# Optimization experiments

Measured on AMD Instinct MI355X. Metric: run time of the kernel, lower is better.

## Reference

```python
import jax, jax.numpy as jnp
import numpy as np

B, T, D_MODEL, N_HEAD = 2, 2048, 1024, 16
HEAD_DIM = D_MODEL // N_HEAD


def setup_inputs() -> dict:
    key = jax.random.key(0)
    ks = jax.random.split(key, 4)
    s = 0.02
    return {
        "x": jax.random.normal(ks[0], (B, T, D_MODEL), dtype=jnp.float32),
        "freqs_cis": jnp.zeros((T, HEAD_DIM // 2), dtype=jnp.float32),  # unused under ALiBi
        "Wq": jax.random.normal(ks[1], (D_MODEL, D_MODEL), dtype=jnp.float32) * s,
        "bq": jnp.zeros((D_MODEL,), dtype=jnp.float32),
        "Wkv": jax.random.normal(ks[2], (2 * D_MODEL, D_MODEL), dtype=jnp.float32) * s,
        "bkv": jnp.zeros((2 * D_MODEL,), dtype=jnp.float32),
        "Wo": jax.random.normal(ks[3], (D_MODEL, D_MODEL), dtype=jnp.float32) * s,
        "bo": jnp.zeros((D_MODEL,), dtype=jnp.float32),
    }


def reference(x, freqs_cis, Wq, bq, Wkv, bkv, Wo, bo):
    Bb, Tt, C = x.shape
    H, Dh = N_HEAD, HEAD_DIM
    # projections (torch Linear: x @ W^T + b)
    q = (x @ Wq.T + bq).reshape(Bb, Tt, H, Dh).transpose(0, 2, 1, 3)      # [B,H,T,Dh]
    kv = (x @ Wkv.T + bkv).reshape(Bb, Tt, 2, H, Dh).transpose(2, 0, 3, 1, 4)
    k, v = kv[0], kv[1]                                                    # [B,H,T,Dh]
    scores = jnp.einsum('bhqd,bhkd->bhqk', q, k) * (1.0 / np.sqrt(Dh))
    # ALiBi: linear slopes (1/H ... 1.0), bias = slope * (j - i)
    slopes = jnp.arange(1, H + 1, dtype=jnp.float32) / H                   # [H]
    pos = jnp.arange(Tt, dtype=jnp.float32)
    dist = pos[None, :] - pos[:, None]                                     # [T,T], j - i
    scores = scores + slopes[:, None, None] * dist[None]                   # broadcast over B
    # causal mask (upper triangle -> -inf)
    causal = pos[:, None] >= pos[None, :]                                  # [T,T] keep-mask
    scores = jnp.where(causal[None, None], scores, -jnp.inf)
    attn = jax.nn.softmax(scores, axis=-1)
    y = jnp.einsum('bhqk,bhkd->bhqd', attn, v)                             # [B,H,T,Dh]
    y = y.transpose(0, 2, 1, 3).reshape(Bb, Tt, C)
    return y @ Wo.T + bo
```

## Files before the change

### kernel.cpp

```cpp
#include <hip/hip_runtime.h>

typedef unsigned short u16;
typedef unsigned int u32;
typedef __bf16 bf16x8 __attribute__((ext_vector_type(8)));
typedef unsigned short u16x8 __attribute__((ext_vector_type(8)));
typedef float f32x4 __attribute__((ext_vector_type(4)));

#define KEY(r) ((((r) ^ ((r) >> 3)) & 7) << 3)
#define GP 72
#define VKEY(d) ((((d) >> 3) & 7) << 3)

static __device__ __forceinline__ u16 f2b(float f) {
  union { float f; unsigned u; } x; x.f = f;
  unsigned r = x.u + 0x7FFFu + ((x.u >> 16) & 1u);
  return (u16)(r >> 16);
}

static __device__ __forceinline__ bf16x8 ld_frag(const u16* p) {
  union { u16x8 s; bf16x8 b; } u;
  u.s = *reinterpret_cast<const u16x8*>(p);
  return u.b;
}

__global__ __launch_bounds__(256) void cvt_f32_bf16(const float* __restrict__ in,
                                                    u16* __restrict__ out, int n4) {
  int i = blockIdx.x * 256 + threadIdx.x;
  if (i >= n4) return;
  float4 v = reinterpret_cast<const float4*>(in)[i];
  ushort4 o;
  o.x = f2b(v.x); o.y = f2b(v.y); o.z = f2b(v.z); o.w = f2b(v.w);
  reinterpret_cast<ushort4*>(out)[i] = o;
}

template <bool OUT_BF16, int BN>
static __device__ __forceinline__ void gemm_body(
    const u16* __restrict__ A, const u16* __restrict__ Bt,
    const float* __restrict__ bias, void* __restrict__ outp,
    int N, int K, int row0, int col0, float scale) {
  constexpr int NF = BN / 32;
  __shared__ alignas(16) u16 As[128 * 64];
  __shared__ alignas(16) u16 Bs[BN * 64];
  const int tid = threadIdx.x, wid = tid >> 6, lane = tid & 63;
  const int wr = wid >> 1, wc = wid & 1;
  const int lr = lane >> 3;
  const int lc = (lane & 7) * 8;
  const int frow = lane & 15, fk = (lane >> 4) * 8;
  f32x4 acc[4][NF] = {};

  for (int k0 = 0; k0 < K; k0 += 64) {
    __syncthreads();
#pragma unroll
    for (int t = 0; t < 4; ++t) {
      const int r = wid * 32 + t * 8 + lr;
      __builtin_amdgcn_global_load_lds(
          (const __attribute__((address_space(1))) unsigned int*)(
              A + (size_t)(row0 + r) * K + k0 + (lc ^ KEY(r))),
          (__attribute__((address_space(3))) unsigned int*)(As + (wid * 32 + t * 8) * 64),
          16, 0, 0);
    }
#pragma unroll
    for (int t = 0; t < NF; ++t) {
      const int r = wid * (BN / 4) + t * 8 + lr;
      __builtin_amdgcn_global_load_lds(
          (const __attribute__((address_space(1))) unsigned int*)(
              Bt + (size_t)(col0 + r) * K + k0 + (lc ^ KEY(r))),
          (__attribute__((address_space(3))) unsigned int*)(Bs + (wid * (BN / 4) + t * 8) * 64),
          16, 0, 0);
    }
    __syncthreads();
#pragma unroll
    for (int ks = 0; ks < 2; ++ks) {
      bf16x8 a[4], b[NF];
#pragma unroll
      for (int m = 0; m < 4; ++m) {
        const int r = wr * 64 + m * 16 + frow;
        a[m] = ld_frag(&As[r * 64 + ((ks * 32 + fk) ^ KEY(r))]);
      }
#pragma unroll
      for (int n = 0; n < NF; ++n) {
        const int r = wc * (BN / 2) + n * 16 + frow;
        b[n] = ld_frag(&Bs[r * 64 + ((ks * 32 + fk) ^ KEY(r))]);
      }
#pragma unroll
      for (int m = 0; m < 4; ++m)
#pragma unroll
        for (int n = 0; n < NF; ++n)
          acc[m][n] = __builtin_amdgcn_mfma_f32_16x16x32_bf16(a[m], b[n], acc[m][n], 0, 0, 0);
    }
  }
  const int colL = lane & 15, rb = (lane >> 4) * 4;
#pragma unroll
  for (int n = 0; n < NF; ++n) {
    const int gc = col0 + wc * (BN / 2) + n * 16 + colL;
    const float bv = bias[gc];
#pragma unroll
    for (int m = 0; m < 4; ++m)
#pragma unroll
      for (int r = 0; r < 4; ++r) {
        const int gr = row0 + wr * 64 + m * 16 + rb + r;
        const float v = (acc[m][n][r] + bv) * scale;
        if constexpr (OUT_BF16)
          reinterpret_cast<u16*>(outp)[(size_t)gr * N + gc] = f2b(v);
        else
          reinterpret_cast<float*>(outp)[(size_t)gr * N + gc] = v;
      }
  }
}

__global__ __launch_bounds__(256) void gemm_qkv(
    const u16* __restrict__ xb, const u16* __restrict__ wqb,
    const u16* __restrict__ wkvb, const float* __restrict__ bq,
    const float* __restrict__ bkv, u16* __restrict__ qb, u16* __restrict__ kvb) {
  const int row0 = blockIdx.x * 128;
  const int by = blockIdx.y;
  const u16* Bt; const float* bias; u16* out; int N, col0; float scale;
  if (by < 8) { Bt = wqb;  bias = bq;  out = qb;  N = 1024; col0 = by * 128;      scale = 0.125f; }
  else        { Bt = wkvb; bias = bkv; out = kvb; N = 2048; col0 = (by - 8) * 128; scale = 1.0f; }
  gemm_body<true, 128>(xb, Bt, bias, out, N, 1024, row0, col0, scale);
}

__global__ __launch_bounds__(256) void gemm_o(
    const u16* __restrict__ yb, const u16* __restrict__ wob,
    const float* __restrict__ bo, float* __restrict__ out) {
  gemm_body<false, 64>(yb, wob, bo, out, 1024, 1024, blockIdx.x * 128, blockIdx.y * 64, 1.0f);
}

__global__ __launch_bounds__(256) void attn_kernel(
    const u16* __restrict__ qb,
    const u16* __restrict__ kvb,
    u16* __restrict__ yb,
    int T) {
  const int C = 1024;
  const int bh = blockIdx.x;
  const int qt = (int)gridDim.y - 1 - (int)blockIdx.y;
  const int b = bh >> 4, h = bh & 15;
  const float slope = (float)(h + 1) * 0.0625f;
  const int tid = threadIdx.x, wid = tid >> 6, lane = tid & 63;
  const int qBase = qt * 64;

  __shared__ alignas(16) u16 Ks[64 * GP];
  __shared__ alignas(16) u16 Vt[64 * GP];
  __shared__ alignas(16) u32 Pl[4][16 * 40];

  const int qc = lane & 15;
  const int g  = lane >> 4;
  const int g4 = g * 4;
  const int fk = g * 8;

  const int q_row = qBase + wid * 16 + qc;
  const u16* qp = qb + (size_t)(b * T + q_row) * C + h * 64;
  const bf16x8 aq0 = ld_frag(qp + fk);
  const bf16x8 aq1 = ld_frag(qp + 32 + fk);
  const int qg = q_row;

  float m_q = -1e30f, l_q = 0.f;
  f32x4 accO[4] = {};

  const int sr = tid >> 3;
  const int sc = (tid & 7) * 8;

  for (int kt = 0; kt <= qt; ++kt) {
    const int kBase = kt * 64;
    __syncthreads();
    {
      const size_t g0 = (size_t)(b * T + kBase + sr) * 2048 + h * 64 + sc;
      const size_t g1 = (size_t)(b * T + kBase + sr + 32) * 2048 + h * 64 + sc;
      *reinterpret_cast<int4*>(&Ks[sr * GP + sc]) = *reinterpret_cast<const int4*>(&kvb[g0]);
      *reinterpret_cast<int4*>(&Ks[(sr + 32) * GP + sc]) = *reinterpret_cast<const int4*>(&kvb[g1]);
      int4 v0 = *reinterpret_cast<const int4*>(&kvb[g0 + 1024]);
      int4 v1 = *reinterpret_cast<const int4*>(&kvb[g1 + 1024]);
      const u16* p0 = reinterpret_cast<const u16*>(&v0);
      const u16* p1 = reinterpret_cast<const u16*>(&v1);
      const int kx = VKEY(sc);
#pragma unroll
      for (int j = 0; j < 8; ++j) {
        const int d = sc + j;
        Vt[d * GP + (sr ^ kx)] = p0[j];
        Vt[d * GP + ((sr + 32) ^ kx)] = p1[j];
      }
    }
    __syncthreads();

    f32x4 accS[4] = {};
#pragma unroll
    for (int n = 0; n < 4; ++n) {
      bf16x8 bk0 = ld_frag(&Ks[(n * 16 + qc) * GP + fk]);
      accS[n] = __builtin_amdgcn_mfma_f32_16x16x32_bf16(bk0, aq0, accS[n], 0, 0, 0);
      bf16x8 bk1 = ld_frag(&Ks[(n * 16 + qc) * GP + 32 + fk]);
      accS[n] = __builtin_amdgcn_mfma_f32_16x16x32_bf16(bk1, aq1, accS[n], 0, 0, 0);
    }

    float tmax = -1e30f;
#pragma unroll
    for (int n = 0; n < 4; ++n) {
      const int kgn = kBase + n * 16 + g4;
#pragma unroll
      for (int r = 0; r < 4; ++r) {
        const int kg = kgn + r;
        float v = fmaf(slope, (float)kg, accS[n][r]);
        v = (kg > qg) ? -1e30f : v;
        accS[n][r] = v;
        tmax = fmaxf(tmax, v);
      }
    }
    tmax = fmaxf(tmax, __shfl_xor(tmax, 16));
    tmax = fmaxf(tmax, __shfl_xor(tmax, 32));
    const float newm = fmaxf(m_q, tmax);
    const float corr = __expf(m_q - newm);
    m_q = newm;
    float psum = 0.f;
#pragma unroll
    for (int n = 0; n < 4; ++n)
#pragma unroll
      for (int r = 0; r < 4; ++r) {
        const float p = __expf(accS[n][r] - newm);
        accS[n][r] = p;
        psum += p;
      }
    psum += __shfl_xor(psum, 16);
    psum += __shfl_xor(psum, 32);
    l_q = l_q * corr + psum;

    u32* Pw = &Pl[wid][qc * 40];
#pragma unroll
    for (int n = 0; n < 4; ++n) {
      union { float f; u32 u; } a0, a1, a2, a3;
      a0.f = accS[n][0]; a1.f = accS[n][1]; a2.f = accS[n][2]; a3.f = accS[n][3];
      u32 w0 = (a0.u >> 16) | (a1.u & 0xFFFF0000u);
      u32 w1 = (a2.u >> 16) | (a3.u & 0xFFFF0000u);
      *reinterpret_cast<uint2*>(&Pw[8 * n + 2 * g]) = uint2{w0, w1};
    }

    float corr4[4];
#pragma unroll
    for (int r = 0; r < 4; ++r) corr4[r] = __shfl(corr, g4 + r);
#pragma unroll
    for (int n = 0; n < 4; ++n)
#pragma unroll
      for (int r = 0; r < 4; ++r) accO[n][r] *= corr4[r];

#pragma unroll
    for (int ks = 0; ks < 2; ++ks) {
      uint4 pv4 = *reinterpret_cast<const uint4*>(&Pl[wid][qc * 40 + 16 * ks + g4]);
      union { uint4 q; u16x8 s; bf16x8 bv; } ap; ap.q = pv4;
#pragma unroll
      for (int n = 0; n < 4; ++n) {
        const int d = n * 16 + qc;
        bf16x8 bv = ld_frag(&Vt[d * GP + ((ks * 32 + fk) ^ VKEY(d))]);
        accO[n] = __builtin_amdgcn_mfma_f32_16x16x32_bf16(ap.bv, bv, accO[n], 0, 0, 0);
      }
    }
  }

  float inv4[4];
#pragma unroll
  for (int r = 0; r < 4; ++r) inv4[r] = 1.0f / __shfl(l_q, g4 + r);
#pragma unroll
  for (int r = 0; r < 4; ++r) {
    const int qg2 = qBase + wid * 16 + g4 + r;
    u16* yrow = yb + (size_t)(b * T + qg2) * C + h * 64;
#pragma unroll
    for (int n = 0; n < 4; ++n) yrow[n * 16 + qc] = f2b(accO[n][r] * inv4[r]);
  }
}

extern "C" void kernel_launch(void* const* d_in, const int* in_sizes, int n_in,
                              void* d_out, int out_size, void* d_ws, size_t ws_size,
                              hipStream_t stream) {
  const float* x   = (const float*)d_in[0];
  const float* Wq  = (const float*)d_in[2];
  const float* bq  = (const float*)d_in[3];
  const float* Wkv = (const float*)d_in[4];
  const float* bkv = (const float*)d_in[5];
  const float* Wo  = (const float*)d_in[6];
  const float* bo  = (const float*)d_in[7];
  float* out = (float*)d_out;

  const int B = 2, T = 2048, C = 1024;
  const int M = B * T;

  char* ws = (char*)d_ws;
  u16* xb   = (u16*)(ws + 0);
  u16* wqb  = (u16*)(ws + 8388608);
  u16* wkvb = (u16*)(ws + 10485760);
  u16* wob  = (u16*)(ws + 14680064);
  u16* qb   = (u16*)(ws + 16777216);
  u16* kvb  = (u16*)(ws + 25165824);
  u16* yb   = (u16*)(ws + 41943040);

  cvt_f32_bf16<<<(M * C / 4 + 255) / 256, 256, 0, stream>>>(x, xb, M * C / 4);
  cvt_f32_bf16<<<(C * C / 4 + 255) / 256, 256, 0, stream>>>(Wq, wqb, C * C / 4);
  cvt_f32_bf16<<<(2 * C * C / 4 + 255) / 256, 256, 0, stream>>>(Wkv, wkvb, 2 * C * C / 4);
  cvt_f32_bf16<<<(C * C / 4 + 255) / 256, 256, 0, stream>>>(Wo, wob, C * C / 4);

  gemm_qkv<<<dim3(M / 128, 8 + 16), 256, 0, stream>>>(xb, wqb, wkvb, bq, bkv, qb, kvb);
  attn_kernel<<<dim3(B * 16, T / 64), 256, 0, stream>>>(qb, kvb, yb, T);
  gemm_o<<<dim3(M / 128, C / 64), 256, 0, stream>>>(yb, wob, bo, out);
}
```

Measured before the change: 213.8 us.

## Fuse conversion launches and widen attention KV tiles with register prefetch

The four fp32-to-bf16 conversion launches are merged into one kernel that picks its source and destination by index range. The attention kernel now processes 128 keys per iteration instead of 64, halving the number of barrier/softmax-rescale rounds. It also prefetches the next K/V tile into registers while the current one is computed. This raises register and LDS use, which may lower occupancy, and computes more masked scores on the diagonal tile. It also changes the LDS padding strides for Vt and the P buffer.

Result: slower. 231.8 us (+8.4%).

```diff
diff --git a/kernel.cpp b/kernel.cpp
--- a/kernel.cpp
+++ b/kernel.cpp
@@ -7,7 +7,9 @@
 typedef float f32x4 __attribute__((ext_vector_type(4)));
 
 #define KEY(r) ((((r) ^ ((r) >> 3)) & 7) << 3)
-#define GP 72
+#define GPK 72
+#define GPV 136
+#define PLP 65
 #define VKEY(d) ((((d) >> 3) & 7) << 3)
 
 static __device__ __forceinline__ u16 f2b(float f) {
@@ -22,14 +24,22 @@
   return u.b;
 }
 
-__global__ __launch_bounds__(256) void cvt_f32_bf16(const float* __restrict__ in,
-                                                    u16* __restrict__ out, int n4) {
-  int i = blockIdx.x * 256 + threadIdx.x;
-  if (i >= n4) return;
-  float4 v = reinterpret_cast<const float4*>(in)[i];
+__global__ __launch_bounds__(256) void cvt_all(
+    const float* __restrict__ x, const float* __restrict__ Wq,
+    const float* __restrict__ Wkv, const float* __restrict__ Wo,
+    u16* __restrict__ xb, u16* __restrict__ wqb,
+    u16* __restrict__ wkvb, u16* __restrict__ wob) {
+  const int i = blockIdx.x * 256 + threadIdx.x;
+  const float* in; u16* out; int base;
+  if (i < 1048576)      { in = x;   out = xb;   base = 0; }
+  else if (i < 1310720) { in = Wq;  out = wqb;  base = 1048576; }
+  else if (i < 1835008) { in = Wkv; out = wkvb; base = 1310720; }
+  else                  { in = Wo;  out = wob;  base = 1835008; }
+  const int j = i - base;
+  float4 v = reinterpret_cast<const float4*>(in)[j];
   ushort4 o;
   o.x = f2b(v.x); o.y = f2b(v.y); o.z = f2b(v.z); o.w = f2b(v.w);
-  reinterpret_cast<ushort4*>(out)[i] = o;
+  reinterpret_cast<ushort4*>(out)[j] = o;
 }
 
 template <bool OUT_BF16, int BN>
@@ -138,9 +148,9 @@
   const int tid = threadIdx.x, wid = tid >> 6, lane = tid & 63;
   const int qBase = qt * 64;
 
-  __shared__ alignas(16) u16 Ks[64 * GP];
-  __shared__ alignas(16) u16 Vt[64 * GP];
-  __shared__ alignas(16) u32 Pl[4][16 * 40];
+  __shared__ alignas(16) u16 Ks[128 * GPK];
+  __shared__ alignas(16) u16 Vt[64 * GPV];
+  __shared__ alignas(16) u32 Pl[4][16 * PLP];
 
   const int qc = lane & 15;
   const int g  = lane >> 4;
@@ -158,41 +168,56 @@
 
   const int sr = tid >> 3;
   const int sc = (tid & 7) * 8;
-
-  for (int kt = 0; kt <= qt; ++kt) {
-    const int kBase = kt * 64;
+  const int kx = VKEY(sc);
+
+  const int nt = (qt + 2) >> 1;
+
+  int4 kreg[4], vreg[4];
+#pragma unroll
+  for (int t = 0; t < 4; ++t) {
+    const int r = sr + 32 * t;
+    const size_t gaddr = (size_t)(b * T + r) * 2048 + h * 64 + sc;
+    kreg[t] = *reinterpret_cast<const int4*>(&kvb[gaddr]);
+    vreg[t] = *reinterpret_cast<const int4*>(&kvb[gaddr + 1024]);
+  }
+
+  for (int kt = 0; kt < nt; ++kt) {
+    const int kBase = kt * 128;
     __syncthreads();
-    {
-      const size_t g0 = (size_t)(b * T + kBase + sr) * 2048 + h * 64 + sc;
-      const size_t g1 = (size_t)(b * T + kBase + sr + 32) * 2048 + h * 64 + sc;
-      *reinterpret_cast<int4*>(&Ks[sr * GP + sc]) = *reinterpret_cast<const int4*>(&kvb[g0]);
-      *reinterpret_cast<int4*>(&Ks[(sr + 32) * GP + sc]) = *reinterpret_cast<const int4*>(&kvb[g1]);
-      int4 v0 = *reinterpret_cast<const int4*>(&kvb[g0 + 1024]);
-      int4 v1 = *reinterpret_cast<const int4*>(&kvb[g1 + 1024]);
-      const u16* p0 = reinterpret_cast<const u16*>(&v0);
-      const u16* p1 = reinterpret_cast<const u16*>(&v1);
-      const int kx = VKEY(sc);
+#pragma unroll
+    for (int t = 0; t < 4; ++t) {
+      const int r = sr + 32 * t;
+      *reinterpret_cast<int4*>(&Ks[r * GPK + sc]) = kreg[t];
+      const u16* pv = reinterpret_cast<const u16*>(&vreg[t]);
 #pragma unroll
       for (int j = 0; j < 8; ++j) {
         const int d = sc + j;
-        Vt[d * GP + (sr ^ kx)] = p0[j];
-        Vt[d * GP + ((sr + 32) ^ kx)] = p1[j];
+        Vt[d * GPV + (r ^ kx)] = pv[j];
       }
     }
     __syncthreads();
-
-    f32x4 accS[4] = {};
-#pragma unroll
-    for (int n = 0; n < 4; ++n) {
-      bf16x8 bk0 = ld_frag(&Ks[(n * 16 + qc) * GP + fk]);
+    if (kt + 1 < nt) {
+#pragma unroll
+      for (int t = 0; t < 4; ++t) {
+        const int r = sr + 32 * t;
+        const size_t gaddr = (size_t)(b * T + kBase + 128 + r) * 2048 + h * 64 + sc;
+        kreg[t] = *reinterpret_cast<const int4*>(&kvb[gaddr]);
+        vreg[t] = *reinterpret_cast<const int4*>(&kvb[gaddr + 1024]);
+      }
+    }
+
+    f32x4 accS[8] = {};
+#pragma unroll
+    for (int n = 0; n < 8; ++n) {
+      bf16x8 bk0 = ld_frag(&Ks[(n * 16 + qc) * GPK + fk]);
       accS[n] = __builtin_amdgcn_mfma_f32_16x16x32_bf16(bk0, aq0, accS[n], 0, 0, 0);
-      bf16x8 bk1 = ld_frag(&Ks[(n * 16 + qc) * GP + 32 + fk]);
+      bf16x8 bk1 = ld_frag(&Ks[(n * 16 + qc) * GPK + 32 + fk]);
       accS[n] = __builtin_amdgcn_mfma_f32_16x16x32_bf16(bk1, aq1, accS[n], 0, 0, 0);
     }
 
     float tmax = -1e30f;
 #pragma unroll
-    for (int n = 0; n < 4; ++n) {
+    for (int n = 0; n < 8; ++n) {
       const int kgn = kBase + n * 16 + g4;
 #pragma unroll
       for (int r = 0; r < 4; ++r) {
@@ -210,7 +235,7 @@
     m_q = newm;
     float psum = 0.f;
 #pragma unroll
-    for (int n = 0; n < 4; ++n)
+    for (int n = 0; n < 8; ++n)
 #pragma unroll
       for (int r = 0; r < 4; ++r) {
         const float p = __expf(accS[n][r] - newm);
@@ -221,9 +246,9 @@
     psum += __shfl_xor(psum, 32);
     l_q = l_q * corr + psum;
 
-    u32* Pw = &Pl[wid][qc * 40];
-#pragma unroll
-    for (int n = 0; n < 4; ++n) {
+    u32* Pw = &Pl[wid][qc * PLP];
+#pragma unroll
+    for (int n = 0; n < 8; ++n) {
       union { float f; u32 u; } a0, a1, a2, a3;
       a0.f = accS[n][0]; a1.f = accS[n][1]; a2.f = accS[n][2]; a3.f = accS[n][3];
       u32 w0 = (a0.u >> 16) | (a1.u & 0xFFFF0000u);
@@ -240,13 +265,13 @@
       for (int r = 0; r < 4; ++r) accO[n][r] *= corr4[r];
 
 #pragma unroll
-    for (int ks = 0; ks < 2; ++ks) {
-      uint4 pv4 = *reinterpret_cast<const uint4*>(&Pl[wid][qc * 40 + 16 * ks + g4]);
+    for (int ks = 0; ks < 4; ++ks) {
+      uint4 pv4 = *reinterpret_cast<const uint4*>(&Pl[wid][qc * PLP + 16 * ks + g4]);
       union { uint4 q; u16x8 s; bf16x8 bv; } ap; ap.q = pv4;
 #pragma unroll
       for (int n = 0; n < 4; ++n) {
         const int d = n * 16 + qc;
-        bf16x8 bv = ld_frag(&Vt[d * GP + ((ks * 32 + fk) ^ VKEY(d))]);
+        bf16x8 bv = ld_frag(&Vt[d * GPV + ((ks * 32 + fk) ^ VKEY(d))]);
         accO[n] = __builtin_amdgcn_mfma_f32_16x16x32_bf16(ap.bv, bv, accO[n], 0, 0, 0);
       }
     }
@@ -288,10 +313,7 @@
   u16* kvb  = (u16*)(ws + 25165824);
   u16* yb   = (u16*)(ws + 41943040);
 
-  cvt_f32_bf16<<<(M * C / 4 + 255) / 256, 256, 0, stream>>>(x, xb, M * C / 4);
-  cvt_f32_bf16<<<(C * C / 4 + 255) / 256, 256, 0, stream>>>(Wq, wqb, C * C / 4);
-  cvt_f32_bf16<<<(2 * C * C / 4 + 255) / 256, 256, 0, stream>>>(Wkv, wkvb, 2 * C * C / 4);
-  cvt_f32_bf16<<<(C * C / 4 + 255) / 256, 256, 0, stream>>>(Wo, wob, C * C / 4);
+  cvt_all<<<8192, 256, 0, stream>>>(x, Wq, Wkv, Wo, xb, wqb, wkvb, wob);
 
   gemm_qkv<<<dim3(M / 128, 8 + 16), 256, 0, stream>>>(xb, wqb, wkvb, bq, bkv, qb, kvb);
   attn_kernel<<<dim3(B * 16, T / 64), 256, 0, stream>>>(qb, kvb, yb, T);
```
